# Kernel tuning notes

Hardware: AMD Instinct MI355X
Metric: run time of the kernel (lower is better)

Reference implementation:

```python
import jax, jax.numpy as jnp
import numpy as np

B, S, D = 1, 2048, 4096
H, HKV, HD = 64, 4, 64
REP = H // HKV
EPS = 1e-5
ROPE_BASE = 10000.0


def setup_inputs() -> dict:
    key = jax.random.key(0)
    ks = jax.random.split(key, 6)
    x = jax.random.normal(ks[0], (B, S, D), dtype=jnp.float32)
    wq = jax.random.normal(ks[1], (D, H * HD), dtype=jnp.float32) * 0.02
    wk = jax.random.normal(ks[2], (D, HKV * HD), dtype=jnp.float32) * 0.02
    wv = jax.random.normal(ks[3], (D, HKV * HD), dtype=jnp.float32) * 0.02
    wo = jax.random.normal(ks[4], (H * HD, D), dtype=jnp.float32) * 0.02
    q_norm_w = jnp.ones((HD,), dtype=jnp.float32)
    k_norm_w = jnp.ones((HD,), dtype=jnp.float32)
    # rotary tables: freqs_cis[t, j] = exp(i * t / base^(2j/head_dim))
    inv_freq = 1.0 / (ROPE_BASE ** (np.arange(0, HD, 2, dtype=np.float32) / HD))
    angles = np.arange(S, dtype=np.float32)[:, None] * inv_freq[None, :]  # [S, HD//2]
    freqs_cos = jnp.asarray(np.cos(angles), dtype=jnp.float32)
    freqs_sin = jnp.asarray(np.sin(angles), dtype=jnp.float32)
    return {"x": x, "wq": wq, "wk": wk, "wv": wv, "wo": wo,
            "q_norm_w": q_norm_w, "k_norm_w": k_norm_w,
            "freqs_cos": freqs_cos, "freqs_sin": freqs_sin}


def _rms_norm(x, w):
    # mean-of-squares over last dim (head_dim)
    ms = jnp.mean(jnp.square(x), axis=-1, keepdims=True)
    return w * (x * jax.lax.rsqrt(ms + EPS))


def _rope(x, cos, sin):
    # x: [B, S, nH, HD]; pairs of consecutive channels form complex numbers
    xr = x.reshape(*x.shape[:-1], HD // 2, 2)
    re, im = xr[..., 0], xr[..., 1]
    c = cos[None, :, None, :]  # [1, S, 1, HD//2]
    s = sin[None, :, None, :]
    out = jnp.stack([re * c - im * s, re * s + im * c], axis=-1)
    return out.reshape(x.shape)


def reference(x, wq, wk, wv, wo, q_norm_w, k_norm_w, freqs_cos, freqs_sin):
    bsz, seqlen, _ = x.shape
    xq = (x @ wq).reshape(bsz, seqlen, H, HD)
    xk = (x @ wk).reshape(bsz, seqlen, HKV, HD)
    xv = (x @ wv).reshape(bsz, seqlen, HKV, HD)
    xq = _rms_norm(xq, q_norm_w)
    xk = _rms_norm(xk, k_norm_w)
    xq = _rope(xq, freqs_cos, freqs_sin)
    xk = _rope(xk, freqs_cos, freqs_sin)
    # GQA: q head h maps to kv head h // REP (repeat_interleave semantics)
    q = xq.reshape(bsz, seqlen, HKV, REP, HD)  # [B, Sq, G, R, d]
    scale = 1.0 / jnp.sqrt(jnp.float32(HD))
    scores = jnp.einsum('bqgrd,bkgd->bgrqk', q, xk) * scale  # [B, G, R, Sq, Sk]
    causal = jnp.tril(jnp.ones((seqlen, seqlen), dtype=bool))
    scores = jnp.where(causal[None, None, None], scores, jnp.float32(-jnp.inf))
    probs = jax.nn.softmax(scores, axis=-1)
    out = jnp.einsum('bgrqk,bkgd->bqgrd', probs, xv)  # [B, Sq, G, R, d]
    out = out.reshape(bsz, seqlen, H * HD)
    return out @ wo
```

## Files before the change

### kernel.cpp

```cpp
#include <hip/hip_runtime.h>
#include <hip/hip_bf16.h>

typedef unsigned short u16;
typedef unsigned int   u32;
typedef __attribute__((ext_vector_type(8))) __bf16 bf16x8;
typedef __attribute__((ext_vector_type(4))) float  f32x4;
typedef __attribute__((ext_vector_type(8))) u16    u16x8;
typedef __attribute__((ext_vector_type(4))) u16    u16x4;
typedef __attribute__((ext_vector_type(2))) u32    u32x2;
typedef __attribute__((ext_vector_type(4))) u32    u32x4;

#define S_LEN 2048
#define DMODEL 4096
#define NH 64
#define NKV 4
#define HD 64

__device__ __forceinline__ u16 f2bf(float f) {
  u32 u = __builtin_bit_cast(u32, f);
  u32 r = (u + 0x7FFFu + ((u >> 16) & 1u)) >> 16;
  return (u16)r;
}
__device__ __forceinline__ u16 bfc(float f) {
  return __builtin_bit_cast(u16, (__bf16)f);
}
__device__ __forceinline__ u32 pk2(float lo, float hi) {
  return (u32)bfc(lo) | ((u32)bfc(hi) << 16);
}
__device__ __forceinline__ float bf2f(u16 u) {
  return __builtin_bit_cast(float, (u32)u << 16);
}
__device__ __forceinline__ float ex2(float x) { return __builtin_amdgcn_exp2f(x); }

__device__ __forceinline__ void gll16(const void* g, void* l) {
  __builtin_amdgcn_global_load_lds(
      (__attribute__((address_space(1))) void*)g,
      (__attribute__((address_space(3))) void*)l, 16, 0, 0);
}

__global__ __launch_bounds__(256) void cvt_f32_bf16_v4(const float* __restrict__ in,
                                                       u16* __restrict__ out) {
  const int i = blockIdx.x * 256 + threadIdx.x;
  float4 f = ((const float4*)in)[i];
  u16x4 u = { f2bf(f.x), f2bf(f.y), f2bf(f.z), f2bf(f.w) };
  *(u16x4*)&out[(size_t)i * 4] = u;
}

__global__ __launch_bounds__(256) void tconvs(const float* __restrict__ in, int istride,
                                              u16* __restrict__ out, int R, int C) {
  __shared__ __align__(16) float tile[32][36];
  const int nc = C >> 5;
  const int cb = blockIdx.x % nc, rb = blockIdx.x / nc;
  const int r = threadIdx.x >> 3, c4 = (threadIdx.x & 7) << 2;
  float4 v = *(const float4*)&in[(size_t)(rb * 32 + r) * istride + cb * 32 + c4];
  *(float4*)&tile[r][c4] = v;
  __syncthreads();
  u32x2 pr;
  pr[0] = pk2(tile[c4 + 0][r], tile[c4 + 1][r]);
  pr[1] = pk2(tile[c4 + 2][r], tile[c4 + 3][r]);
  *(u32x2*)&out[(size_t)(cb * 32 + r) * R + rb * 32 + c4] = pr;
}

__global__ __launch_bounds__(256) void tconvs4(const float* __restrict__ in, int istride,
                                               size_t pstr,
                                               u16* __restrict__ out, int R, int C) {
  __shared__ __align__(16) float tile[32][36];
  const int nc = C >> 5;
  const int cb = blockIdx.x % nc, rb = blockIdx.x / nc;
  const int r = threadIdx.x >> 3, c4 = (threadIdx.x & 7) << 2;
  const size_t idx = (size_t)(rb * 32 + r) * istride + cb * 32 + c4;
  float4 v = *(const float4*)&in[idx];
#pragma unroll
  for (int j = 1; j < 4; ++j) {
    float4 u = *(const float4*)&in[idx + j * pstr];
    v.x += u.x; v.y += u.y; v.z += u.z; v.w += u.w;
  }
  *(float4*)&tile[r][c4] = v;
  __syncthreads();
  u32x2 pr;
  pr[0] = pk2(tile[c4 + 0][r], tile[c4 + 1][r]);
  pr[1] = pk2(tile[c4 + 2][r], tile[c4 + 3][r]);
  *(u32x2*)&out[(size_t)(cb * 32 + r) * R + rb * 32 + c4] = pr;
}

__global__ __launch_bounds__(256) void norm_rope_q(const u16* __restrict__ in,
                                                   int in_stride, int nheads,
                                                   const float* __restrict__ nw,
                                                   const float* __restrict__ cosT,
                                                   const float* __restrict__ sinT,
                                                   u16* __restrict__ outp, int out_stride,
                                                   float oscale) {
  const int wid = blockIdx.x * 4 + (threadIdx.x >> 6);
  const int l = threadIdx.x & 63;
  const int s = wid / nheads, h = wid - s * nheads;
  const size_t idx = (size_t)s * in_stride + h * 64 + l;
  const float v = bf2f(in[idx]);
  float sq = v * v;
#pragma unroll
  for (int off = 32; off; off >>= 1) sq += __shfl_xor(sq, off, 64);
  const float rr = rsqrtf(sq * (1.f / 64.f) + 1e-5f);
  const float vn = v * rr * nw[l];
  const float p = __shfl_xor(vn, 1, 64);
  const int i2 = l >> 1;
  const float c = cosT[(size_t)s * 32 + i2];
  const float sn = sinT[(size_t)s * 32 + i2];
  const float o = ((l & 1) ? fmaf(p, sn, vn * c) : fmaf(-p, sn, vn * c)) * oscale;
  outp[(size_t)s * out_stride + h * 64 + l] = f2bf(o);
}

__global__ __launch_bounds__(256) void norm_rope_k4(const float* __restrict__ in,
                                                    size_t pstr,
                                                    int in_stride, int nheads,
                                                    const float* __restrict__ nw,
                                                    const float* __restrict__ cosT,
                                                    const float* __restrict__ sinT,
                                                    u16* __restrict__ outp, int out_stride,
                                                    float oscale) {
  const int wid = blockIdx.x * 4 + (threadIdx.x >> 6);
  const int l = threadIdx.x & 63;
  const int s = wid / nheads, h = wid - s * nheads;
  const size_t idx = (size_t)s * in_stride + h * 64 + l;
  float v = in[idx];
#pragma unroll
  for (int j = 1; j < 4; ++j) v += in[idx + j * pstr];
  float sq = v * v;
#pragma unroll
  for (int off = 32; off; off >>= 1) sq += __shfl_xor(sq, off, 64);
  const float rr = rsqrtf(sq * (1.f / 64.f) + 1e-5f);
  const float vn = v * rr * nw[l];
  const float p = __shfl_xor(vn, 1, 64);
  const int i2 = l >> 1;
  const float c = cosT[(size_t)s * 32 + i2];
  const float sn = sinT[(size_t)s * 32 + i2];
  const float o = ((l & 1) ? fmaf(p, sn, vn * c) : fmaf(-p, sn, vn * c)) * oscale;
  outp[(size_t)s * out_stride + h * 64 + l] = f2bf(o);
}

__global__ __launch_bounds__(256) void gemm_kv(const u16* __restrict__ A,
                                               const u16* __restrict__ Bt,
                                               float* __restrict__ C, size_t pstr,
                                               int M, int N, int K) {
  __shared__ __align__(16) u16 As[128 * 32];
  __shared__ __align__(16) u16 Bs[128 * 32];
  int bid = blockIdx.x;
  const int cpx = gridDim.x >> 3;
  bid = (bid & 7) * cpx + (bid >> 3);
  const int nbn = N >> 7;
  const int pertile = (M >> 7) * nbn;
  const int sl = bid / pertile;
  const int rem = bid - sl * pertile;
  const int bm = rem / nbn, bn = rem % nbn;
  const int m0 = bm << 7, n0 = bn << 7;
  const int tid = threadIdx.x;
  const int w = tid >> 6, l = tid & 63;
  const int wr = w >> 1, wc = w & 1;
  f32x4 acc[4][4] = {};

  const int Kq = K >> 2;
  const int kbase = sl * Kq;

  const char* Ag = (const char*)A +
      ((size_t)(m0 + w * 32 + (l >> 2)) * K + kbase + (l & 3) * 8) * 2;
  const char* Bg = (const char*)Bt +
      ((size_t)(n0 + w * 32 + (l >> 2)) * K + kbase + (l & 3) * 8) * 2;
  char* Al = (char*)As + (w * 32) * 64;
  char* Bl = (char*)Bs + (w * 32) * 64;
  const size_t rowadv = (size_t)16 * K * 2;

  for (int k0 = 0; k0 < Kq; k0 += 32) {
    gll16(Ag, Al);
    gll16(Ag + rowadv, Al + 1024);
    gll16(Bg, Bl);
    gll16(Bg + rowadv, Bl + 1024);
    Ag += 64; Bg += 64;
    __syncthreads();
    bf16x8 af[4], bq[4];
#pragma unroll
    for (int i = 0; i < 4; ++i) {
      af[i] = *(const bf16x8*)&As[(wr * 64 + i * 16 + (l & 15)) * 32 + (l >> 4) * 8];
      bq[i] = *(const bf16x8*)&Bs[(wc * 64 + i * 16 + (l & 15)) * 32 + (l >> 4) * 8];
    }
#pragma unroll
    for (int mi = 0; mi < 4; ++mi)
#pragma unroll
      for (int ni = 0; ni < 4; ++ni)
        acc[mi][ni] = __builtin_amdgcn_mfma_f32_16x16x32_bf16(af[mi], bq[ni], acc[mi][ni], 0, 0, 0);
    __syncthreads();
  }
  float* Cs = C + sl * pstr;
  const int r0 = (l >> 4) * 4, c0 = l & 15;
#pragma unroll
  for (int mi = 0; mi < 4; ++mi)
#pragma unroll
    for (int ni = 0; ni < 4; ++ni)
#pragma unroll
      for (int r = 0; r < 4; ++r)
        Cs[(size_t)(m0 + wr * 64 + mi * 16 + r0 + r) * N + (n0 + wc * 64 + ni * 16 + c0)] =
            acc[mi][ni][r];
}

template <int BF16OUT>
__global__ __launch_bounds__(512) void gemm_mn(const u16* __restrict__ A,
                                               const u16* __restrict__ Bt,
                                               void* __restrict__ Cout,
                                               int M, int N, int K) {
  extern __shared__ __align__(16) char lds[];
  int bid = blockIdx.x;
  const int cpx = gridDim.x >> 3;
  bid = (bid & 7) * cpx + (bid >> 3);
  const int nbn = N >> 7;
  const int bm = bid / nbn, bn = bid % nbn;
  const int m0 = bm << 8, n0 = bn << 7;
  const int t = threadIdx.x, w = t >> 6, l = t & 63;
  const int wr = w >> 1, wc = w & 1;
  const int lr = l & 15, lg = l >> 4;

  const int sR = t >> 3, slot = t & 7;
  const int su = slot ^ (sR & 7);
  const int d1 = sR * 128 + slot * 16;
  const u16* Ag = A + (size_t)(m0 + 2 * sR + (su >> 2)) * K + (su & 3) * 8;
  const u16* Bg = Bt + (size_t)(n0 + 2 * sR + (su >> 2)) * K + (su & 3) * 8;
  const size_t r128 = (size_t)128 * K;

  f32x4 acc[4][4] = {};
  const int NPH = K >> 5;

  auto stage = [&](int ph) {
    const int kofs = ph * 32;
    char* pb = lds + (ph & 3) * 24576;
    gll16(Ag + kofs, pb + d1);
    gll16(Ag + r128 + kofs, pb + 8192 + d1);
    gll16(Bg + kofs, pb + 16384 + d1);
  };
  stage(0);
  stage(1);
  stage(2);

  const int sfrag = ((lr & 1) << 2) | lg;
  const int swz = (sfrag ^ ((lr >> 1) & 7)) << 4;
  const int aoff = (wr * 32 + (lr >> 1)) * 128 + swz;
  const int boff = 16384 + (wc * 32 + (lr >> 1)) * 128 + swz;

  bf16x8 a[4], b[4];
  auto read_frags = [&](int ph) {
    const char* base = lds + (ph & 3) * 24576;
#pragma unroll
    for (int mf = 0; mf < 4; ++mf) a[mf] = *(const bf16x8*)(base + aoff + mf * 1024);
#pragma unroll
    for (int nf = 0; nf < 4; ++nf) b[nf] = *(const bf16x8*)(base + boff + nf * 1024);
  };
  auto mfma16 = [&]() {
    __builtin_amdgcn_s_setprio(1);
#pragma unroll
    for (int mf = 0; mf < 4; ++mf)
#pragma unroll
      for (int nf = 0; nf < 4; ++nf)
        acc[mf][nf] = __builtin_amdgcn_mfma_f32_16x16x32_bf16(a[mf], b[nf], acc[mf][nf], 0, 0, 0);
    __builtin_amdgcn_s_setprio(0);
    asm volatile("" ::: "memory");
  };

#define GSYNC(NW) __builtin_amdgcn_sched_barrier(0); \
  asm volatile("s_waitcnt vmcnt(" #NW ")" ::: "memory"); \
  __builtin_amdgcn_s_barrier(); \
  __builtin_amdgcn_sched_barrier(0);

  GSYNC(6)
  read_frags(0);

  for (int ph = 0; ph < NPH - 3; ++ph) {
    __builtin_amdgcn_sched_barrier(0);
    stage(ph + 3);
    mfma16();
    GSYNC(6)
    read_frags(ph + 1);
  }
  __builtin_amdgcn_sched_barrier(0);
  mfma16();
  GSYNC(3)
  read_frags(NPH - 2);
  __builtin_amdgcn_sched_barrier(0);
  mfma16();
  GSYNC(0)
  read_frags(NPH - 1);
  __builtin_amdgcn_sched_barrier(0);
  mfma16();
#undef GSYNC

#pragma unroll
  for (int mf = 0; mf < 4; ++mf)
#pragma unroll
    for (int nf = 0; nf < 4; ++nf)
#pragma unroll
      for (int rr = 0; rr < 4; ++rr) {
        const size_t cidx = (size_t)(m0 + wr * 64 + mf * 16 + lg * 4 + rr) * N +
                            (n0 + wc * 64 + nf * 16 + lr);
        if (BF16OUT)
          ((u16*)Cout)[cidx] = bfc(acc[mf][nf][rr]);
        else
          ((float*)Cout)[cidx] = acc[mf][nf][rr];
      }
}

__global__ __launch_bounds__(256) void attn_fwd(const u16* __restrict__ Q,
                                                const u16* __restrict__ Kb,
                                                const u16* __restrict__ VT,
                                                u16* __restrict__ O) {
  const int h = blockIdx.x & 63;
  const int qb = (S_LEN / 64 - 1) - (blockIdx.x >> 6);
  const int kvh = h >> 4;
  __shared__ __align__(16) char KV[2 * 16384];
  const int tid = threadIdx.x;
  const int w = tid >> 6, l = tid & 63;
  const int lr = l & 15, lg = l >> 4;

  const int srow = w * 16 + (l >> 3);
  const int s0 = (l & 7) ^ (srow & 7);
  const int sv = (s0 & 4) | ((s0 & 1) << 1) | ((s0 & 2) >> 1);
  const char* Kg = (const char*)Kb + kvh * 128 + (size_t)srow * 512 + s0 * 16;
  const char* Vg = (const char*)VT + (size_t)(kvh * 64 + srow) * (S_LEN * 2) + sv * 16;
  const int wofs = w * 2048;

  auto stage = [&](int page) {
    char* pb = KV + page * 16384 + wofs;
    gll16(Kg, pb);
    gll16(Kg + 8 * 512, pb + 1024);
    gll16(Vg, pb + 8192);
    gll16(Vg + 8 * (S_LEN * 2), pb + 8192 + 1024);
    Kg += 64 * 512;
    Vg += 128;
  };

  bf16x8 qf[2];
  {
    const size_t qoff = (size_t)(qb * 64 + w * 16 + lr) * DMODEL + h * HD + lg * 8;
    qf[0] = *(const bf16x8*)&Q[qoff];
    qf[1] = *(const bf16x8*)&Q[qoff + 32];
  }
  f32x4 o[4] = {};
  float lrow = 0.f;
  const int qlane = qb * 64 + w * 16 + lr;
  const int abase = (l & 48) | ((l >> 2) & 12);

  const int xr = lr & 7;
  const int kb0 = lr * 128 + ((lg ^ xr) << 4);
  const int kb1 = lr * 128 + (((4 + lg) ^ xr) << 4);
  const int vb0 = 8192 + kb0;
  const int vb1 = 8192 + kb1;

  stage(0);

  for (int t = 0; t <= qb; ++t) {
    __builtin_amdgcn_sched_barrier(0);
    asm volatile("s_waitcnt vmcnt(0)" ::: "memory");
    __builtin_amdgcn_s_barrier();
    __builtin_amdgcn_sched_barrier(0);
    if (t < qb) stage((t + 1) & 1);
    const char* page = KV + (t & 1) * 16384;

    f32x4 sf[4] = {};
    __builtin_amdgcn_s_setprio(1);
#pragma unroll
    for (int ni = 0; ni < 4; ++ni) {
      bf16x8 kf0 = *(const bf16x8*)(page + kb0 + ni * 2048);
      bf16x8 kf1 = *(const bf16x8*)(page + kb1 + ni * 2048);
      sf[ni] = __builtin_amdgcn_mfma_f32_16x16x32_bf16(kf0, qf[0], sf[ni], 0, 0, 0);
      sf[ni] = __builtin_amdgcn_mfma_f32_16x16x32_bf16(kf1, qf[1], sf[ni], 0, 0, 0);
    }
    __builtin_amdgcn_s_setprio(0);
    if (t == qb) {
      const int kvb = t * 64 + lg * 4;
#pragma unroll
      for (int ni = 0; ni < 4; ++ni)
#pragma unroll
        for (int r = 0; r < 4; ++r)
          if (kvb + ni * 16 + r > qlane) sf[ni][r] = -1e30f;
    }
    float p[4][4];
    float r4[4];
#pragma unroll
    for (int ni = 0; ni < 4; ++ni) {
#pragma unroll
      for (int r = 0; r < 4; ++r) p[ni][r] = ex2(sf[ni][r]);
      r4[ni] = (p[ni][0] + p[ni][1]) + (p[ni][2] + p[ni][3]);
    }
    float rs = (r4[0] + r4[1]) + (r4[2] + r4[3]);
    rs += __shfl_xor(rs, 16, 64);
    rs += __shfl_xor(rs, 32, 64);
    lrow += rs;

    const bool odd = (lg & 1);
#pragma unroll
    for (int kk = 0; kk < 2; ++kk) {
      const int nA = 2 * kk, nB = 2 * kk + 1;
      const u32 cA0 = pk2(p[nA][0], p[nA][1]), cA1 = pk2(p[nA][2], p[nA][3]);
      const u32 cB0 = pk2(p[nB][0], p[nB][1]), cB1 = pk2(p[nB][2], p[nB][3]);
      const u32 cS0 = odd ? cB0 : cA0, cS1 = odd ? cB1 : cA1;
      const u32 cP0 = odd ? cA0 : cB0, cP1 = odd ? cA1 : cB1;
      const u32 rP0 = (u32)__shfl_xor((int)cP0, 16, 64);
      const u32 rP1 = (u32)__shfl_xor((int)cP1, 16, 64);
      u32x4 wv;
      wv[0] = odd ? rP0 : cS0;
      wv[1] = odd ? rP1 : cS1;
      wv[2] = odd ? cS0 : rP0;
      wv[3] = odd ? cS1 : rP1;
      const bf16x8 pa = __builtin_bit_cast(bf16x8, wv);
      const int vb = kk ? vb1 : vb0;
      __builtin_amdgcn_s_setprio(1);
#pragma unroll
      for (int ni = 0; ni < 4; ++ni) {
        bf16x8 vf = *(const bf16x8*)(page + vb + ni * 2048);
        o[ni] = __builtin_amdgcn_mfma_f32_16x16x32_bf16(pa, vf, o[ni], 0, 0, 0);
      }
      __builtin_amdgcn_s_setprio(0);
    }
  }
  const float lv0 = __shfl(lrow, abase + 0, 64);
  const float lv1 = __shfl(lrow, abase + 1, 64);
  const float lv2 = __shfl(lrow, abase + 2, 64);
  const float lv3 = __shfl(lrow, abase + 3, 64);
  const f32x4 lv = {lv0, lv1, lv2, lv3};
#pragma unroll
  for (int ni = 0; ni < 4; ++ni)
#pragma unroll
    for (int r = 0; r < 4; ++r) {
      const size_t orow = (size_t)(qb * 64 + w * 16 + lg * 4 + r);
      O[orow * DMODEL + h * HD + ni * 16 + lr] = f2bf(o[ni][r] / lv[r]);
    }
}

extern "C" void kernel_launch(void* const* d_in, const int* in_sizes, int n_in,
                              void* d_out, int out_size, void* d_ws, size_t ws_size,
                              hipStream_t stream) {
  const float* x   = (const float*)d_in[0];
  const float* wq  = (const float*)d_in[1];
  const float* wk  = (const float*)d_in[2];
  const float* wv  = (const float*)d_in[3];
  const float* wo  = (const float*)d_in[4];
  const float* qnw = (const float*)d_in[5];
  const float* knw = (const float*)d_in[6];
  const float* fc  = (const float*)d_in[7];
  const float* fs  = (const float*)d_in[8];
  float* out = (float*)d_out;

  char* ws = (char*)d_ws;
  size_t off = 0;
  auto alloc = [&](size_t bytes) {
    char* p = ws + off;
    off += (bytes + 255) & ~(size_t)255;
    return p;
  };
  const size_t KVP = (size_t)S_LEN * 512;
  u16*   xb    = (u16*)alloc((size_t)S_LEN * DMODEL * 2);
  u16*   wqT   = (u16*)alloc((size_t)DMODEL * DMODEL * 2);
  u16*   wkvT  = (u16*)alloc((size_t)512 * DMODEL * 2);
  u16*   woT   = (u16*)alloc((size_t)DMODEL * DMODEL * 2);
  u16*   Pq    = (u16*)alloc((size_t)S_LEN * DMODEL * 2);
  float* KVf   = (float*)alloc(KVP * 4 * 4);
  u16*   Qn    = (u16*)alloc((size_t)S_LEN * DMODEL * 2);
  u16*   Kn    = (u16*)alloc((size_t)S_LEN * 256 * 2);
  u16*   VTb   = (u16*)alloc((size_t)256 * S_LEN * 2);
  u16*   Ob    = (u16*)alloc((size_t)S_LEN * DMODEL * 2);

  hipFuncSetAttribute((const void*)gemm_mn<1>, hipFuncAttributeMaxDynamicSharedMemorySize, 98304);
  hipFuncSetAttribute((const void*)gemm_mn<0>, hipFuncAttributeMaxDynamicSharedMemorySize, 98304);

  cvt_f32_bf16_v4<<<(S_LEN * DMODEL / 4) / 256, 256, 0, stream>>>(x, xb);
  tconvs<<<(4096 / 32) * (4096 / 32), 256, 0, stream>>>(wq, 4096, wqT, 4096, 4096);
  tconvs<<<(4096 / 32) * (256 / 32), 256, 0, stream>>>(wk, 256, wkvT, 4096, 256);
  tconvs<<<(4096 / 32) * (256 / 32), 256, 0, stream>>>(wv, 256,
      wkvT + (size_t)256 * 4096, 4096, 256);
  tconvs<<<(4096 / 32) * (4096 / 32), 256, 0, stream>>>(wo, 4096, woT, 4096, 4096);

  gemm_mn<1><<<(2048 / 256) * (4096 / 128), 512, 98304, stream>>>(
      xb, wqT, Pq, 2048, 4096, 4096);
  gemm_kv<<<4 * (2048 / 128) * (512 / 128), 256, 0, stream>>>(
      xb, wkvT, KVf, KVP, 2048, 512, 4096);

  const float QSCALE = 0.125f * 1.44269504088896340736f;
  norm_rope_q<<<(S_LEN * NH) / 4, 256, 0, stream>>>(Pq, DMODEL, NH, qnw, fc, fs,
                                                    Qn, DMODEL, QSCALE);
  norm_rope_k4<<<(S_LEN * NKV) / 4, 256, 0, stream>>>(KVf, KVP, 512, NKV,
                                                      knw, fc, fs, Kn, 256, 1.0f);
  tconvs4<<<(2048 / 32) * (256 / 32), 256, 0, stream>>>(KVf + 256, 512, KVP,
                                                        VTb, 2048, 256);

  attn_fwd<<<(S_LEN / 64) * NH, 256, 0, stream>>>(Qn, Kn, VTb, Ob);

  gemm_mn<0><<<(2048 / 256) * (4096 / 128), 512, 98304, stream>>>(
      Ob, woT, out, 2048, 4096, 4096);
}
```

Before: 316.2 us.

## Shrink GEMM pipeline to three LDS stages for two blocks per CU

The large bf16 GEMM goes from a four-buffer, three-ahead prefetch pipeline (96KB LDS) to a three-buffer, two-ahead pipeline (72KB LDS). The main loop is unrolled by three with fixed buffer indices, and fragment reads now happen inside each compute step instead of being prefetched across the barrier. launch_bounds(512,2) together with the smaller LDS footprint aims to fit two 512-thread blocks per CU for more latency hiding. In exchange, prefetch depth and LDS-read/MFMA overlap within a wave are reduced, and the loop count is hardcoded to K=4096.

```diff
diff --git a/kernel.cpp b/kernel.cpp
--- a/kernel.cpp
+++ b/kernel.cpp
@@ -200,10 +200,10 @@
 }
 
 template <int BF16OUT>
-__global__ __launch_bounds__(512) void gemm_mn(const u16* __restrict__ A,
-                                               const u16* __restrict__ Bt,
-                                               void* __restrict__ Cout,
-                                               int M, int N, int K) {
+__global__ __launch_bounds__(512, 2) void gemm_mn(const u16* __restrict__ A,
+                                                  const u16* __restrict__ Bt,
+                                                  void* __restrict__ Cout,
+                                                  int M, int N, int K) {
   extern __shared__ __align__(16) char lds[];
   int bid = blockIdx.x;
   const int cpx = gridDim.x >> 3;
@@ -223,33 +223,29 @@
   const size_t r128 = (size_t)128 * K;
 
   f32x4 acc[4][4] = {};
-  const int NPH = K >> 5;
-
-  auto stage = [&](int ph) {
+
+  auto stage = [&](int ph, const int pg) {
     const int kofs = ph * 32;
-    char* pb = lds + (ph & 3) * 24576;
+    char* pb = lds + pg * 24576;
     gll16(Ag + kofs, pb + d1);
     gll16(Ag + r128 + kofs, pb + 8192 + d1);
     gll16(Bg + kofs, pb + 16384 + d1);
   };
-  stage(0);
-  stage(1);
-  stage(2);
+  stage(0, 0);
+  stage(1, 1);
 
   const int sfrag = ((lr & 1) << 2) | lg;
   const int swz = (sfrag ^ ((lr >> 1) & 7)) << 4;
   const int aoff = (wr * 32 + (lr >> 1)) * 128 + swz;
   const int boff = 16384 + (wc * 32 + (lr >> 1)) * 128 + swz;
 
-  bf16x8 a[4], b[4];
-  auto read_frags = [&](int ph) {
-    const char* base = lds + (ph & 3) * 24576;
+  auto compute = [&](const int pg) {
+    const char* base = lds + pg * 24576;
+    bf16x8 a[4], b[4];
 #pragma unroll
     for (int mf = 0; mf < 4; ++mf) a[mf] = *(const bf16x8*)(base + aoff + mf * 1024);
 #pragma unroll
     for (int nf = 0; nf < 4; ++nf) b[nf] = *(const bf16x8*)(base + boff + nf * 1024);
-  };
-  auto mfma16 = [&]() {
     __builtin_amdgcn_s_setprio(1);
 #pragma unroll
     for (int mf = 0; mf < 4; ++mf)
@@ -260,32 +256,24 @@
     asm volatile("" ::: "memory");
   };
 
-#define GSYNC(NW) __builtin_amdgcn_sched_barrier(0); \
-  asm volatile("s_waitcnt vmcnt(" #NW ")" ::: "memory"); \
+#define SYNC3 __builtin_amdgcn_sched_barrier(0); \
+  asm volatile("s_waitcnt vmcnt(3)" ::: "memory"); \
   __builtin_amdgcn_s_barrier(); \
   __builtin_amdgcn_sched_barrier(0);
-
-  GSYNC(6)
-  read_frags(0);
-
-  for (int ph = 0; ph < NPH - 3; ++ph) {
-    __builtin_amdgcn_sched_barrier(0);
-    stage(ph + 3);
-    mfma16();
-    GSYNC(6)
-    read_frags(ph + 1);
+#define SYNC0 __builtin_amdgcn_sched_barrier(0); \
+  asm volatile("s_waitcnt vmcnt(0)" ::: "memory"); \
+  __builtin_amdgcn_s_barrier(); \
+  __builtin_amdgcn_sched_barrier(0);
+
+  for (int b = 0; b < 126; b += 3) {
+    SYNC3; stage(b + 2, 2); compute(0);
+    SYNC3; stage(b + 3, 0); compute(1);
+    SYNC3; stage(b + 4, 1); compute(2);
   }
-  __builtin_amdgcn_sched_barrier(0);
-  mfma16();
-  GSYNC(3)
-  read_frags(NPH - 2);
-  __builtin_amdgcn_sched_barrier(0);
-  mfma16();
-  GSYNC(0)
-  read_frags(NPH - 1);
-  __builtin_amdgcn_sched_barrier(0);
-  mfma16();
-#undef GSYNC
+  SYNC3; compute(0);
+  SYNC0; compute(1);
+#undef SYNC3
+#undef SYNC0
 
 #pragma unroll
   for (int mf = 0; mf < 4; ++mf)
@@ -462,8 +450,8 @@
   u16*   VTb   = (u16*)alloc((size_t)256 * S_LEN * 2);
   u16*   Ob    = (u16*)alloc((size_t)S_LEN * DMODEL * 2);
 
-  hipFuncSetAttribute((const void*)gemm_mn<1>, hipFuncAttributeMaxDynamicSharedMemorySize, 98304);
-  hipFuncSetAttribute((const void*)gemm_mn<0>, hipFuncAttributeMaxDynamicSharedMemorySize, 98304);
+  hipFuncSetAttribute((const void*)gemm_mn<1>, hipFuncAttributeMaxDynamicSharedMemorySize, 73728);
+  hipFuncSetAttribute((const void*)gemm_mn<0>, hipFuncAttributeMaxDynamicSharedMemorySize, 73728);
 
   cvt_f32_bf16_v4<<<(S_LEN * DMODEL / 4) / 256, 256, 0, stream>>>(x, xb);
   tconvs<<<(4096 / 32) * (4096 / 32), 256, 0, stream>>>(wq, 4096, wqT, 4096, 4096);
@@ -472,7 +460,7 @@
       wkvT + (size_t)256 * 4096, 4096, 256);
   tconvs<<<(4096 / 32) * (4096 / 32), 256, 0, stream>>>(wo, 4096, woT, 4096, 4096);
 
-  gemm_mn<1><<<(2048 / 256) * (4096 / 128), 512, 98304, stream>>>(
+  gemm_mn<1><<<(2048 / 256) * (4096 / 128), 512, 73728, stream>>>(
       xb, wqT, Pq, 2048, 4096, 4096);
   gemm_kv<<<4 * (2048 / 128) * (512 / 128), 256, 0, stream>>>(
       xb, wkvT, KVf, KVP, 2048, 512, 4096);
@@ -487,6 +475,6 @@
 
   attn_fwd<<<(S_LEN / 64) * NH, 256, 0, stream>>>(Qn, Kn, VTb, Ob);
 
-  gemm_mn<0><<<(2048 / 256) * (4096 / 128), 512, 98304, stream>>>(
+  gemm_mn<0><<<(2048 / 256) * (4096 / 128), 512, 73728, stream>>>(
       Ob, woT, out, 2048, 4096, 4096);
 }
```

Result: slower. 323.8 us (+2.4%).

## Fuse Q RMSNorm+RoPE into attention and process two heads per block

Applied to the files above, without the earlier changes.

Removes the separate norm_rope_q kernel and applies Q normalization, rotary embedding and scaling inside the attention kernel when loading Q fragments. Each attention block now handles two query heads sharing the same KV head, so every K/V tile staged in shared memory is reused twice. This removes a kernel launch and a full round trip of the Q tensor through memory, and halves the K/V load traffic. In exchange the grid is half as large and each thread holds more registers, which may lower occupancy.

```diff
diff --git a/kernel.cpp b/kernel.cpp
--- a/kernel.cpp
+++ b/kernel.cpp
@@ -81,31 +81,6 @@
   pr[0] = pk2(tile[c4 + 0][r], tile[c4 + 1][r]);
   pr[1] = pk2(tile[c4 + 2][r], tile[c4 + 3][r]);
   *(u32x2*)&out[(size_t)(cb * 32 + r) * R + rb * 32 + c4] = pr;
-}
-
-__global__ __launch_bounds__(256) void norm_rope_q(const u16* __restrict__ in,
-                                                   int in_stride, int nheads,
-                                                   const float* __restrict__ nw,
-                                                   const float* __restrict__ cosT,
-                                                   const float* __restrict__ sinT,
-                                                   u16* __restrict__ outp, int out_stride,
-                                                   float oscale) {
-  const int wid = blockIdx.x * 4 + (threadIdx.x >> 6);
-  const int l = threadIdx.x & 63;
-  const int s = wid / nheads, h = wid - s * nheads;
-  const size_t idx = (size_t)s * in_stride + h * 64 + l;
-  const float v = bf2f(in[idx]);
-  float sq = v * v;
-#pragma unroll
-  for (int off = 32; off; off >>= 1) sq += __shfl_xor(sq, off, 64);
-  const float rr = rsqrtf(sq * (1.f / 64.f) + 1e-5f);
-  const float vn = v * rr * nw[l];
-  const float p = __shfl_xor(vn, 1, 64);
-  const int i2 = l >> 1;
-  const float c = cosT[(size_t)s * 32 + i2];
-  const float sn = sinT[(size_t)s * 32 + i2];
-  const float o = ((l & 1) ? fmaf(p, sn, vn * c) : fmaf(-p, sn, vn * c)) * oscale;
-  outp[(size_t)s * out_stride + h * 64 + l] = f2bf(o);
 }
 
 __global__ __launch_bounds__(256) void norm_rope_k4(const float* __restrict__ in,
@@ -302,13 +277,17 @@
       }
 }
 
-__global__ __launch_bounds__(256) void attn_fwd(const u16* __restrict__ Q,
+__global__ __launch_bounds__(256) void attn_fwd(const u16* __restrict__ Qp,
                                                 const u16* __restrict__ Kb,
                                                 const u16* __restrict__ VT,
+                                                const float* __restrict__ nw,
+                                                const float* __restrict__ cosT,
+                                                const float* __restrict__ sinT,
                                                 u16* __restrict__ O) {
-  const int h = blockIdx.x & 63;
-  const int qb = (S_LEN / 64 - 1) - (blockIdx.x >> 6);
-  const int kvh = h >> 4;
+  const int hp = blockIdx.x & 31;
+  const int qb = (S_LEN / 64 - 1) - (blockIdx.x >> 5);
+  const int h0 = hp << 1;
+  const int kvh = h0 >> 4;
   __shared__ __align__(16) char KV[2 * 16384];
   const int tid = threadIdx.x;
   const int w = tid >> 6, l = tid & 63;
@@ -331,15 +310,58 @@
     Vg += 128;
   };
 
-  bf16x8 qf[2];
-  {
-    const size_t qoff = (size_t)(qb * 64 + w * 16 + lr) * DMODEL + h * HD + lg * 8;
-    qf[0] = *(const bf16x8*)&Q[qoff];
-    qf[1] = *(const bf16x8*)&Q[qoff + 32];
+  const int qrow = qb * 64 + w * 16 + lr;
+
+  float cv[8], sn_[8], nv[16];
+#pragma unroll
+  for (int jj = 0; jj < 4; ++jj) {
+    cv[jj]      = cosT[(size_t)qrow * 32 + lg * 4 + jj];
+    sn_[jj]     = sinT[(size_t)qrow * 32 + lg * 4 + jj];
+    cv[4 + jj]  = cosT[(size_t)qrow * 32 + 16 + lg * 4 + jj];
+    sn_[4 + jj] = sinT[(size_t)qrow * 32 + 16 + lg * 4 + jj];
   }
-  f32x4 o[4] = {};
-  float lrow = 0.f;
-  const int qlane = qb * 64 + w * 16 + lr;
+#pragma unroll
+  for (int j = 0; j < 8; ++j) {
+    nv[j]     = nw[lg * 8 + j];
+    nv[8 + j] = nw[32 + lg * 8 + j];
+  }
+  const float QSCALE = 0.125f * 1.44269504088896340736f;
+
+  auto mkq = [&](int h, bf16x8* qf) {
+    const size_t qoff = (size_t)qrow * DMODEL + h * HD + lg * 8;
+    u16x8 r0 = *(const u16x8*)&Qp[qoff];
+    u16x8 r1 = *(const u16x8*)&Qp[qoff + 32];
+    float v[16];
+    float sq = 0.f;
+#pragma unroll
+    for (int j = 0; j < 8; ++j) {
+      v[j] = bf2f(r0[j]);
+      v[8 + j] = bf2f(r1[j]);
+      sq = fmaf(v[j], v[j], sq);
+      sq = fmaf(v[8 + j], v[8 + j], sq);
+    }
+    sq += __shfl_xor(sq, 16, 64);
+    sq += __shfl_xor(sq, 32, 64);
+    const float rr = rsqrtf(sq * (1.f / 64.f) + 1e-5f) * QSCALE;
+    u32x4 w0, w1;
+#pragma unroll
+    for (int jj = 0; jj < 4; ++jj) {
+      const float re0 = v[2 * jj] * nv[2 * jj] * rr;
+      const float im0 = v[2 * jj + 1] * nv[2 * jj + 1] * rr;
+      w0[jj] = pk2(re0 * cv[jj] - im0 * sn_[jj], re0 * sn_[jj] + im0 * cv[jj]);
+      const float re1 = v[8 + 2 * jj] * nv[8 + 2 * jj] * rr;
+      const float im1 = v[8 + 2 * jj + 1] * nv[8 + 2 * jj + 1] * rr;
+      w1[jj] = pk2(re1 * cv[4 + jj] - im1 * sn_[4 + jj], re1 * sn_[4 + jj] + im1 * cv[4 + jj]);
+    }
+    qf[0] = __builtin_bit_cast(bf16x8, w0);
+    qf[1] = __builtin_bit_cast(bf16x8, w1);
+  };
+  bf16x8 qfA[2], qfB[2];
+  mkq(h0, qfA);
+  mkq(h0 + 1, qfB);
+
+  f32x4 oA[4] = {}, oB[4] = {};
+  float lrowA = 0.f, lrowB = 0.f;
   const int abase = (l & 48) | ((l >> 2) & 12);
 
   const int xr = lr & 7;
@@ -348,16 +370,8 @@
   const int vb0 = 8192 + kb0;
   const int vb1 = 8192 + kb1;
 
-  stage(0);
-
-  for (int t = 0; t <= qb; ++t) {
-    __builtin_amdgcn_sched_barrier(0);
-    asm volatile("s_waitcnt vmcnt(0)" ::: "memory");
-    __builtin_amdgcn_s_barrier();
-    __builtin_amdgcn_sched_barrier(0);
-    if (t < qb) stage((t + 1) & 1);
-    const char* page = KV + (t & 1) * 16384;
-
+  auto proc = [&](const char* page, const bf16x8* qf, f32x4* o, float& lrow, bool diag,
+                  int t) {
     f32x4 sf[4] = {};
     __builtin_amdgcn_s_setprio(1);
 #pragma unroll
@@ -368,13 +382,13 @@
       sf[ni] = __builtin_amdgcn_mfma_f32_16x16x32_bf16(kf1, qf[1], sf[ni], 0, 0, 0);
     }
     __builtin_amdgcn_s_setprio(0);
-    if (t == qb) {
+    if (diag) {
       const int kvb = t * 64 + lg * 4;
 #pragma unroll
       for (int ni = 0; ni < 4; ++ni)
 #pragma unroll
         for (int r = 0; r < 4; ++r)
-          if (kvb + ni * 16 + r > qlane) sf[ni][r] = -1e30f;
+          if (kvb + ni * 16 + r > qrow) sf[ni][r] = -1e30f;
     }
     float p[4][4];
     float r4[4];
@@ -414,19 +428,38 @@
       }
       __builtin_amdgcn_s_setprio(0);
     }
+  };
+
+  stage(0);
+
+  for (int t = 0; t <= qb; ++t) {
+    __builtin_amdgcn_sched_barrier(0);
+    asm volatile("s_waitcnt vmcnt(0)" ::: "memory");
+    __builtin_amdgcn_s_barrier();
+    __builtin_amdgcn_sched_barrier(0);
+    if (t < qb) stage((t + 1) & 1);
+    const char* page = KV + (t & 1) * 16384;
+    const bool diag = (t == qb);
+    proc(page, qfA, oA, lrowA, diag, t);
+    proc(page, qfB, oB, lrowB, diag, t);
   }
-  const float lv0 = __shfl(lrow, abase + 0, 64);
-  const float lv1 = __shfl(lrow, abase + 1, 64);
-  const float lv2 = __shfl(lrow, abase + 2, 64);
-  const float lv3 = __shfl(lrow, abase + 3, 64);
-  const f32x4 lv = {lv0, lv1, lv2, lv3};
-#pragma unroll
-  for (int ni = 0; ni < 4; ++ni)
-#pragma unroll
-    for (int r = 0; r < 4; ++r) {
-      const size_t orow = (size_t)(qb * 64 + w * 16 + lg * 4 + r);
-      O[orow * DMODEL + h * HD + ni * 16 + lr] = f2bf(o[ni][r] / lv[r]);
-    }
+
+  auto fin = [&](const f32x4* o, float lrow, int h) {
+    const float lv0 = __shfl(lrow, abase + 0, 64);
+    const float lv1 = __shfl(lrow, abase + 1, 64);
+    const float lv2 = __shfl(lrow, abase + 2, 64);
+    const float lv3 = __shfl(lrow, abase + 3, 64);
+    const f32x4 lv = {lv0, lv1, lv2, lv3};
+#pragma unroll
+    for (int ni = 0; ni < 4; ++ni)
+#pragma unroll
+      for (int r = 0; r < 4; ++r) {
+        const size_t orow = (size_t)(qb * 64 + w * 16 + lg * 4 + r);
+        O[orow * DMODEL + h * HD + ni * 16 + lr] = f2bf(o[ni][r] / lv[r]);
+      }
+  };
+  fin(oA, lrowA, h0);
+  fin(oB, lrowB, h0 + 1);
 }
 
 extern "C" void kernel_launch(void* const* d_in, const int* in_sizes, int n_in,
@@ -457,7 +490,6 @@
   u16*   woT   = (u16*)alloc((size_t)DMODEL * DMODEL * 2);
   u16*   Pq    = (u16*)alloc((size_t)S_LEN * DMODEL * 2);
   float* KVf   = (float*)alloc(KVP * 4 * 4);
-  u16*   Qn    = (u16*)alloc((size_t)S_LEN * DMODEL * 2);
   u16*   Kn    = (u16*)alloc((size_t)S_LEN * 256 * 2);
   u16*   VTb   = (u16*)alloc((size_t)256 * S_LEN * 2);
   u16*   Ob    = (u16*)alloc((size_t)S_LEN * DMODEL * 2);
@@ -477,15 +509,12 @@
   gemm_kv<<<4 * (2048 / 128) * (512 / 128), 256, 0, stream>>>(
       xb, wkvT, KVf, KVP, 2048, 512, 4096);
 
-  const float QSCALE = 0.125f * 1.44269504088896340736f;
-  norm_rope_q<<<(S_LEN * NH) / 4, 256, 0, stream>>>(Pq, DMODEL, NH, qnw, fc, fs,
-                                                    Qn, DMODEL, QSCALE);
   norm_rope_k4<<<(S_LEN * NKV) / 4, 256, 0, stream>>>(KVf, KVP, 512, NKV,
                                                       knw, fc, fs, Kn, 256, 1.0f);
   tconvs4<<<(2048 / 32) * (256 / 32), 256, 0, stream>>>(KVf + 256, 512, KVP,
                                                         VTb, 2048, 256);
 
-  attn_fwd<<<(S_LEN / 64) * NH, 256, 0, stream>>>(Qn, Kn, VTb, Ob);
+  attn_fwd<<<(S_LEN / 64) * (NH / 2), 256, 0, stream>>>(Pq, Kn, VTb, qnw, fc, fs, Ob);
 
   gemm_mn<0><<<(2048 / 256) * (4096 / 128), 512, 98304, stream>>>(
       Ob, woT, out, 2048, 4096, 4096);
```

After: 293.4 us. 7.2% less time.
